# Kernel tuning notes

Hardware: AMD Instinct MI355X
Metric: run time of the kernel (lower is better)

## Reference

```python
import jax, jax.numpy as jnp
import numpy as np

N = 50000          # total particles (nodes)
E = 800000         # num edges
D = 256            # embed_dim
H = 8              # num_heads
ED = 6             # edge_dim
HD = D // H // 2   # head_dim = 16
LAMBDA_INIT = 1.0 - float(np.exp(-1.0))  # lambda_init_fn(depth=1)


def setup_inputs() -> dict:
    key = jax.random.key(0)
    ks = jax.random.split(key, 9)
    sc = lambda k, shape, fan_in: jax.random.normal(k, shape, jnp.float32) * (fan_in ** -0.5)
    x = jax.random.normal(ks[0], (N, D), jnp.float32)
    edge_index = jax.random.randint(ks[1], (2, E), 0, N, dtype=jnp.int64)
    edge_attr = jax.random.normal(ks[2], (E, ED), jnp.float32)
    v_w = sc(ks[3], (D, D), D)
    out_w = sc(ks[4], (D, D), D)
    e_w1 = sc(ks[5], (D, ED), ED)
    e_b1 = jnp.zeros((D,), jnp.float32)
    e_w2 = sc(ks[6], (2 * H, D), D)
    e_b2 = jnp.zeros((2 * H,), jnp.float32)
    lambda_q1 = 0.1 * jax.random.normal(ks[7], (100,), jnp.float32)
    lambda_k1 = 0.1 * jax.random.normal(ks[8], (100,), jnp.float32)
    return {"x": x, "edge_attr": edge_attr, "v_w": v_w, "out_w": out_w,
            "e_w1": e_w1, "e_b1": e_b1, "e_w2": e_w2, "e_b2": e_b2,
            "lambda_q1": lambda_q1, "lambda_k1": lambda_k1,
            "edge_index": edge_index}


def _scatter_softmax(scores, tgt, n):
    # numerically-stable segment softmax over edges grouped by tgt node
    m = jax.ops.segment_max(scores, tgt, num_segments=n)      # [n, H]
    e = jnp.exp(scores - m[tgt])                              # [E, H]
    s = jax.ops.segment_sum(e, tgt, num_segments=n)           # [n, H]
    return e / s[tgt]


def reference(x, edge_attr, v_w, out_w, e_w1, e_b1, e_w2, e_b2,
              lambda_q1, lambda_k1, edge_index):
    src, tgt = edge_index[0], edge_index[1]
    # V projection (no bias), split into heads of size 2*head_dim
    V = (x @ v_w.T).reshape(N, H, 2 * HD)
    # edge encoder MLP: Linear -> GELU(exact) -> Linear
    h = jax.nn.gelu(edge_attr @ e_w1.T + e_b1, approximate=False)
    edge_scores = (h @ e_w2.T + e_b2).reshape(E, H, 2)
    a1 = _scatter_softmax(edge_scores[:, :, 0], tgt, N)
    a2 = _scatter_softmax(edge_scores[:, :, 1], tgt, N)
    lambda_1 = jnp.exp(jnp.sum(lambda_q1 * lambda_k1))
    beta = jax.nn.sigmoid(lambda_1 * LAMBDA_INIT)
    attn_weights = a1 - beta * a2                              # [E, H]
    weighted_V = attn_weights[:, :, None] * V[src]             # [E, H, 2*HD]
    out = jax.ops.segment_sum(weighted_V, tgt, num_segments=N).reshape(N, D)
    out = out @ out_w.T
    return out, attn_weights, beta
```

## Files before the change

### kernel.cpp

```cpp
#include <hip/hip_runtime.h>
#include <hip/hip_bf16.h>
#include <math.h>

#define N_NODES 50000
#define N_EDGES 800000
#define DIM 256
#define HEADS 8
#define LAMBDA_INIT 0.63212055882855767f

using bf16x8 = __attribute__((ext_vector_type(8))) short;
using bf16x4 = __attribute__((ext_vector_type(4))) short;
using f32x4  = __attribute__((ext_vector_type(4))) float;
using f32x2  = __attribute__((ext_vector_type(2))) float;
#define MFMA16(a, b, c) __builtin_amdgcn_mfma_f32_16x16x32_bf16(a, b, c, 0, 0, 0)

__device__ __forceinline__ short f2b(float f) {
    __hip_bfloat16 h = __float2bfloat16(f);
    return *reinterpret_cast<short*>(&h);
}
__device__ __forceinline__ float b2f(short s) {
    unsigned u = ((unsigned)(unsigned short)s) << 16;
    return __uint_as_float(u);
}
__device__ __forceinline__ unsigned cvt_pk_bf16(float a, float b) {
    unsigned r;
    asm("v_cvt_pk_bf16_f32 %0, %1, %2" : "=v"(r) : "v"(a), "v"(b));
    return r;
}

__device__ __forceinline__ float gelu_f(float x) {
    float az = 0.70710678118654752f * fabsf(x);
    float t  = __builtin_amdgcn_rcpf(fmaf(0.47047f, az, 1.f));
    float q  = fmaf(fmaf(0.3739278f, t, -0.0479399f), t, 0.1740121f) * t;
    float E  = __expf(-az * az);
    return fmaf(-q * E, fabsf(x), fmaxf(x, 0.f));
}

__global__ __launch_bounds__(256) void scan1(const int* __restrict__ cnt,
                                             int* __restrict__ offs,
                                             int* __restrict__ partials, int n) {
    __shared__ int sh[256];
    int i = blockIdx.x * 256 + threadIdx.x;
    int v = (i < n) ? cnt[i] : 0;
    sh[threadIdx.x] = v;
    __syncthreads();
    for (int s = 1; s < 256; s <<= 1) {
        int add = (threadIdx.x >= s) ? sh[threadIdx.x - s] : 0;
        __syncthreads();
        sh[threadIdx.x] += add;
        __syncthreads();
    }
    if (i < n) offs[i] = sh[threadIdx.x] - v;
    if (threadIdx.x == 255) partials[blockIdx.x] = sh[255];
}

__global__ __launch_bounds__(256) void scan2(int* __restrict__ partials, int nb,
                                             const float* __restrict__ lq,
                                             const float* __restrict__ lk,
                                             float* __restrict__ beta_ws,
                                             float* __restrict__ beta_out) {
    __shared__ int sh[256];
    __shared__ float redb[128];
    int tid = threadIdx.x;
    int v = (tid < nb) ? partials[tid] : 0;
    sh[tid] = v;
    __syncthreads();
    for (int s = 1; s < 256; s <<= 1) {
        int add = (tid >= s) ? sh[tid - s] : 0;
        __syncthreads();
        sh[tid] += add;
        __syncthreads();
    }
    if (tid < nb) partials[tid] = sh[tid] - v;

    if (tid < 128) {
        float b = 0.f;
        for (int i = tid; i < 100; i += 128) b += lq[i] * lk[i];
        redb[tid] = b;
    }
    __syncthreads();
    for (int s = 64; s > 0; s >>= 1) {
        if (tid < s) redb[tid] += redb[tid + s];
        __syncthreads();
    }
    if (tid == 0) {
        float l1 = expf(redb[0]);
        float b = 1.f / (1.f + expf(-l1 * LAMBDA_INIT));
        *beta_ws = b;
        *beta_out = b;
    }
}

__global__ __launch_bounds__(256) void scan3(int* __restrict__ offs,
                                             const int* __restrict__ partials,
                                             int* __restrict__ cursor, int n) {
    int i = blockIdx.x * 256 + threadIdx.x;
    if (i < n) {
        int o = offs[i] + partials[blockIdx.x];
        offs[i] = o;
        cursor[i] = o;
    }
    if (i == 0) offs[n] = N_EDGES;
}

__global__ __launch_bounds__(256) void scatter_eid(const int* __restrict__ tgt,
                                                   int* __restrict__ cursor,
                                                   int* __restrict__ sorted_eid) {
    int e = blockIdx.x * 256 + threadIdx.x;
    if (e < N_EDGES) {
        int p = atomicAdd(&cursor[tgt[e]], 1);
        sorted_eid[p] = e;
    }
}

template <bool ABF, bool CBF>
__global__ __launch_bounds__(256) void gemm_mfma_t(const void* __restrict__ Av,
                                                   const float* __restrict__ W,
                                                   void* __restrict__ Cv, int M) {
    __shared__ __align__(16) short As[128 * 40];
    __shared__ __align__(16) short Ws[64 * 40];
    int tid = threadIdx.x;
    int lane = tid & 63, wv = tid >> 6;
    int l16 = lane & 15, quad = lane >> 4;
    int bm = blockIdx.x * 128, bn = blockIdx.y * 64;

    f32x4 acc[2][4];
#pragma unroll
    for (int mt = 0; mt < 2; ++mt)
#pragma unroll
        for (int nt = 0; nt < 4; ++nt) acc[mt][nt] = (f32x4){0.f, 0.f, 0.f, 0.f};

    int r = tid >> 1, hf = tid & 1;
    int rw = (tid & 127) >> 1, hw = tid & 1;

    for (int k0 = 0; k0 < 256; k0 += 32) {
        {
            int m = bm + r;
            bf16x8 p0, p1;
            if (ABF) {
                if (m < M) {
                    const bf16x8* ap =
                        (const bf16x8*)&((const short*)Av)[(size_t)m * 256 + k0 + hf * 16];
                    p0 = ap[0]; p1 = ap[1];
                } else {
                    p0 = (bf16x8){0,0,0,0,0,0,0,0}; p1 = p0;
                }
            } else {
                float4 f0, f1, f2, f3;
                if (m < M) {
                    const float4* ap =
                        (const float4*)&((const float*)Av)[(size_t)m * 256 + k0 + hf * 16];
                    f0 = ap[0]; f1 = ap[1]; f2 = ap[2]; f3 = ap[3];
                } else {
                    f0 = f1 = f2 = f3 = make_float4(0.f, 0.f, 0.f, 0.f);
                }
                p0[0]=f2b(f0.x); p0[1]=f2b(f0.y); p0[2]=f2b(f0.z); p0[3]=f2b(f0.w);
                p0[4]=f2b(f1.x); p0[5]=f2b(f1.y); p0[6]=f2b(f1.z); p0[7]=f2b(f1.w);
                p1[0]=f2b(f2.x); p1[1]=f2b(f2.y); p1[2]=f2b(f2.z); p1[3]=f2b(f2.w);
                p1[4]=f2b(f3.x); p1[5]=f2b(f3.y); p1[6]=f2b(f3.z); p1[7]=f2b(f3.w);
            }
            *(bf16x8*)&As[r * 40 + hf * 16]     = p0;
            *(bf16x8*)&As[r * 40 + hf * 16 + 8] = p1;
        }
        if (tid < 128) {
            const float4* wp = (const float4*)&W[(size_t)(bn + rw) * 256 + k0 + hw * 16];
            float4 f0 = wp[0], f1 = wp[1], f2 = wp[2], f3 = wp[3];
            bf16x8 p0, p1;
            p0[0]=f2b(f0.x); p0[1]=f2b(f0.y); p0[2]=f2b(f0.z); p0[3]=f2b(f0.w);
            p0[4]=f2b(f1.x); p0[5]=f2b(f1.y); p0[6]=f2b(f1.z); p0[7]=f2b(f1.w);
            p1[0]=f2b(f2.x); p1[1]=f2b(f2.y); p1[2]=f2b(f2.z); p1[3]=f2b(f2.w);
            p1[4]=f2b(f3.x); p1[5]=f2b(f3.y); p1[6]=f2b(f3.z); p1[7]=f2b(f3.w);
            *(bf16x8*)&Ws[rw * 40 + hw * 16]     = p0;
            *(bf16x8*)&Ws[rw * 40 + hw * 16 + 8] = p1;
        }
        __syncthreads();
#pragma unroll
        for (int mt = 0; mt < 2; ++mt) {
            bf16x8 afr = *(bf16x8*)&As[(wv * 32 + mt * 16 + l16) * 40 + quad * 8];
#pragma unroll
            for (int nt = 0; nt < 4; ++nt) {
                bf16x8 bfr = *(bf16x8*)&Ws[(nt * 16 + l16) * 40 + quad * 8];
                acc[mt][nt] = MFMA16(afr, bfr, acc[mt][nt]);
            }
        }
        __syncthreads();
    }
#pragma unroll
    for (int mt = 0; mt < 2; ++mt) {
#pragma unroll
        for (int rr = 0; rr < 4; ++rr) {
            int m = bm + wv * 32 + mt * 16 + quad * 4 + rr;
            if (m < M) {
#pragma unroll
                for (int nt = 0; nt < 4; ++nt) {
                    if (CBF)
                        ((short*)Cv)[(size_t)m * 256 + bn + nt * 16 + l16] =
                            f2b(acc[mt][nt][rr]);
                    else
                        ((float*)Cv)[(size_t)m * 256 + bn + nt * 16 + l16] =
                            acc[mt][nt][rr];
                }
            }
        }
    }
}

__global__ __launch_bounds__(256) void edge_mlp_mfma(const float* __restrict__ edge_attr,
                                                     const float* __restrict__ e_w1,
                                                     const float* __restrict__ e_b1,
                                                     const float* __restrict__ e_w2,
                                                     const float* __restrict__ e_b2,
                                                     float* __restrict__ scores,
                                                     const int* __restrict__ tgt,
                                                     int* __restrict__ cnt) {
    __shared__ __align__(16) short w1s[256 * 8];
    __shared__ __align__(16) float b1s[256];
    __shared__ __align__(16) float ea_s[256 * 6];

    int tid = threadIdx.x;
    int lane = tid & 63, wv = tid >> 6;
    int l16 = lane & 15, quad = lane >> 4;

    atomicAdd(&cnt[tgt[blockIdx.x * 256 + tid]], 1);

    {
        int n = tid;
#pragma unroll
        for (int k = 0; k < 6; ++k) w1s[n * 8 + k] = f2b(e_w1[n * 6 + k]);
        w1s[n * 8 + 6] = 0; w1s[n * 8 + 7] = 0;
        b1s[n] = e_b1[n];
    }
    {
        size_t base = (size_t)blockIdx.x * (256 * 6);
#pragma unroll
        for (int it = 0; it < 6; ++it) {
            int i = tid + it * 256;
            ea_s[i] = edge_attr[base + i];
        }
    }

    bf16x8 w2f[8];
#pragma unroll
    for (int c = 0; c < 8; ++c) {
#pragma unroll
        for (int j = 0; j < 8; ++j) {
            int col = c * 32 + ((j & 4) ? 16 : 0) + quad * 4 + (j & 3);
            w2f[c][j] = f2b(e_w2[l16 * 256 + col]);
        }
    }
    float b2r = e_b2[l16];
    __syncthreads();

    bf16x8 bfr[4];
#pragma unroll
    for (int g = 0; g < 4; ++g) {
        bfr[g] = (bf16x8){0, 0, 0, 0, 0, 0, 0, 0};
        if (quad == 0) {
            const float* p = &ea_s[(wv * 64 + g * 16 + l16) * 6];
#pragma unroll
            for (int j = 0; j < 6; ++j) bfr[g][j] = f2b(p[j]);
        }
    }

    f32x4 acc[4];
#pragma unroll
    for (int g = 0; g < 4; ++g) acc[g] = (f32x4){0.f, 0.f, 0.f, 0.f};

#pragma unroll
    for (int c2 = 0; c2 < 8; ++c2) {
        bf16x8 af0 = (bf16x8){0, 0, 0, 0, 0, 0, 0, 0};
        bf16x8 af1 = (bf16x8){0, 0, 0, 0, 0, 0, 0, 0};
        if (quad == 0) {
            af0 = *(bf16x8*)&w1s[((2 * c2) * 16 + l16) * 8];
            af1 = *(bf16x8*)&w1s[((2 * c2 + 1) * 16 + l16) * 8];
        }
        f32x4 bb0 = *(const f32x4*)&b1s[(2 * c2) * 16 + quad * 4];
        f32x4 bb1 = *(const f32x4*)&b1s[(2 * c2 + 1) * 16 + quad * 4];
#pragma unroll
        for (int g = 0; g < 4; ++g) {
            f32x4 cc0 = MFMA16(af0, bfr[g], bb0);
            f32x4 cc1 = MFMA16(af1, bfr[g], bb1);
            unsigned pw[4];
            pw[0] = cvt_pk_bf16(gelu_f(cc0[0]), gelu_f(cc0[1]));
            pw[1] = cvt_pk_bf16(gelu_f(cc0[2]), gelu_f(cc0[3]));
            pw[2] = cvt_pk_bf16(gelu_f(cc1[0]), gelu_f(cc1[1]));
            pw[3] = cvt_pk_bf16(gelu_f(cc1[2]), gelu_f(cc1[3]));
            bf16x8 pa = *reinterpret_cast<bf16x8*>(pw);
            acc[g] = MFMA16(pa, w2f[c2], acc[g]);
        }
    }

    long eblk = (long)blockIdx.x * 256 + wv * 64;
#pragma unroll
    for (int g = 0; g < 4; ++g) {
        long e0 = eblk + g * 16;
#pragma unroll
        for (int rr = 0; rr < 4; ++rr)
            scores[(size_t)(e0 + quad * 4 + rr) * 16 + l16] = acc[g][rr] + b2r;
    }
}

__global__ __launch_bounds__(256) void node_agg3(const int* __restrict__ sorted_eid,
                                                 const int* __restrict__ offs,
                                                 const int* __restrict__ srcp,
                                                 const float* __restrict__ scores,
                                                 const short* __restrict__ Vb,
                                                 const float* __restrict__ betap,
                                                 short* __restrict__ accumb,
                                                 float* __restrict__ attn_out) {
    __shared__ __align__(16) float scr_all[4][16 * 65];
    __shared__ __align__(16) float ms_all[4][32];
    __shared__ int src_all[4][64];

    int tid = threadIdx.x;
    int wv = tid >> 6, lane = tid & 63;
    int n = blockIdx.x * 4 + wv;
    float* scr = scr_all[wv];
    float* ms  = ms_all[wv];
    int* srcs  = src_all[wv];

    int beg = offs[n];
    int deg = offs[n + 1] - beg;
    int c16 = lane & 15, q4 = lane >> 4;
    int d0 = lane * 4, hh = lane >> 3;

    if (deg == 0) {
        bf16x4 z = (bf16x4){0, 0, 0, 0};
        *(bf16x4*)&accumb[(size_t)n * 256 + d0] = z;
        return;
    }
    float beta = *betap;

    if (deg <= 64) {
        int k = lane;
        int eid = 0, src = 0;
        float sc[16];
        if (k < deg) {
            eid = sorted_eid[beg + k];
            src = srcp[eid];
            const f32x4* sp = (const f32x4*)&scores[(size_t)eid * 16];
            f32x4 s0 = sp[0], s1 = sp[1], s2 = sp[2], s3 = sp[3];
            sc[0]=s0[0]; sc[1]=s0[1]; sc[2]=s0[2]; sc[3]=s0[3];
            sc[4]=s1[0]; sc[5]=s1[1]; sc[6]=s1[2]; sc[7]=s1[3];
            sc[8]=s2[0]; sc[9]=s2[1]; sc[10]=s2[2]; sc[11]=s2[3];
            sc[12]=s3[0]; sc[13]=s3[1]; sc[14]=s3[2]; sc[15]=s3[3];
        } else {
#pragma unroll
            for (int c = 0; c < 16; ++c) sc[c] = -INFINITY;
        }
        srcs[k] = src;
#pragma unroll
        for (int c = 0; c < 16; ++c) scr[c * 65 + k] = sc[c];

        float mloc = -INFINITY;
        for (int j = 0; 4 * j < deg; ++j)
            mloc = fmaxf(mloc, scr[c16 * 65 + 4 * j + q4]);
        mloc = fmaxf(mloc, __shfl_xor(mloc, 16));
        mloc = fmaxf(mloc, __shfl_xor(mloc, 32));
        float sloc = 0.f;
        for (int j = 0; 4 * j < deg; ++j)
            sloc += __expf(scr[c16 * 65 + 4 * j + q4] - mloc);
        sloc += __shfl_xor(sloc, 16);
        sloc += __shfl_xor(sloc, 32);
        if (lane < 16) {
            ms[c16] = mloc;
            ms[16 + c16] = __builtin_amdgcn_rcpf(sloc);
        }

        if (k < deg) {
            float w[8];
#pragma unroll
            for (int h = 0; h < 8; ++h) {
                f32x2 mp = *(const f32x2*)&ms[2 * h];
                f32x2 rp = *(const f32x2*)&ms[16 + 2 * h];
                w[h] = __expf(sc[2 * h] - mp[0]) * rp[0]
                     - beta * __expf(sc[2 * h + 1] - mp[1]) * rp[1];
            }
            f32x4 w0 = (f32x4){w[0], w[1], w[2], w[3]};
            f32x4 w1 = (f32x4){w[4], w[5], w[6], w[7]};
            *(f32x4*)&attn_out[(size_t)eid * 8]     = w0;
            *(f32x4*)&attn_out[(size_t)eid * 8 + 4] = w1;
            *(f32x4*)&scr[k * 8]     = w0;
            *(f32x4*)&scr[k * 8 + 4] = w1;
        }

        float a0 = 0.f, a1 = 0.f, a2 = 0.f, a3 = 0.f;
        for (int kk = 0; kk < deg; ++kk) {
            float wk = scr[kk * 8 + hh];
            int sk = srcs[kk];
            bf16x4 v = *(const bf16x4*)&Vb[(size_t)sk * 256 + d0];
            a0 += wk * b2f(v[0]);
            a1 += wk * b2f(v[1]);
            a2 += wk * b2f(v[2]);
            a3 += wk * b2f(v[3]);
        }
        bf16x4 r;
        r[0] = f2b(a0); r[1] = f2b(a1); r[2] = f2b(a2); r[3] = f2b(a3);
        *(bf16x4*)&accumb[(size_t)n * 256 + d0] = r;
        return;
    }

    float m_run = -INFINITY, s_run = 0.f;
    for (int base = 0; base < deg; base += 64) {
        int k = base + lane;
        float sc[16];
        if (k < deg) {
            int eid = sorted_eid[beg + k];
            const f32x4* sp = (const f32x4*)&scores[(size_t)eid * 16];
            f32x4 s0 = sp[0], s1 = sp[1], s2 = sp[2], s3 = sp[3];
            sc[0]=s0[0]; sc[1]=s0[1]; sc[2]=s0[2]; sc[3]=s0[3];
            sc[4]=s1[0]; sc[5]=s1[1]; sc[6]=s1[2]; sc[7]=s1[3];
            sc[8]=s2[0]; sc[9]=s2[1]; sc[10]=s2[2]; sc[11]=s2[3];
            sc[12]=s3[0]; sc[13]=s3[1]; sc[14]=s3[2]; sc[15]=s3[3];
        } else {
#pragma unroll
            for (int c = 0; c < 16; ++c) sc[c] = -INFINITY;
        }
#pragma unroll
        for (int c = 0; c < 16; ++c) scr[c * 65 + lane] = sc[c];
        float mc = -INFINITY;
#pragma unroll
        for (int j = 0; j < 16; ++j)
            mc = fmaxf(mc, scr[c16 * 65 + 4 * j + q4]);
        mc = fmaxf(mc, __shfl_xor(mc, 16));
        mc = fmaxf(mc, __shfl_xor(mc, 32));
        float m_new = fmaxf(m_run, mc);
        float ssum = 0.f;
#pragma unroll
        for (int j = 0; j < 16; ++j)
            ssum += __expf(scr[c16 * 65 + 4 * j + q4] - m_new);
        ssum += __shfl_xor(ssum, 16);
        ssum += __shfl_xor(ssum, 32);
        s_run = s_run * __expf(m_run - m_new) + ssum;
        m_run = m_new;
    }
    if (lane < 16) {
        ms[c16] = m_run;
        ms[16 + c16] = __builtin_amdgcn_rcpf(s_run);
    }

    float a0 = 0.f, a1 = 0.f, a2 = 0.f, a3 = 0.f;
    for (int base = 0; base < deg; base += 64) {
        int k = base + lane;
        int cn = min(64, deg - base);
        int src = 0;
        if (lane < cn) {
            int eid = sorted_eid[beg + k];
            src = srcp[eid];
            const f32x4* sp = (const f32x4*)&scores[(size_t)eid * 16];
            f32x4 s0 = sp[0], s1 = sp[1], s2 = sp[2], s3 = sp[3];
            float sc[16];
            sc[0]=s0[0]; sc[1]=s0[1]; sc[2]=s0[2]; sc[3]=s0[3];
            sc[4]=s1[0]; sc[5]=s1[1]; sc[6]=s1[2]; sc[7]=s1[3];
            sc[8]=s2[0]; sc[9]=s2[1]; sc[10]=s2[2]; sc[11]=s2[3];
            sc[12]=s3[0]; sc[13]=s3[1]; sc[14]=s3[2]; sc[15]=s3[3];
            float w[8];
#pragma unroll
            for (int h = 0; h < 8; ++h) {
                f32x2 mp = *(const f32x2*)&ms[2 * h];
                f32x2 rp = *(const f32x2*)&ms[16 + 2 * h];
                w[h] = __expf(sc[2 * h] - mp[0]) * rp[0]
                     - beta * __expf(sc[2 * h + 1] - mp[1]) * rp[1];
            }
            f32x4 w0 = (f32x4){w[0], w[1], w[2], w[3]};
            f32x4 w1 = (f32x4){w[4], w[5], w[6], w[7]};
            *(f32x4*)&attn_out[(size_t)eid * 8]     = w0;
            *(f32x4*)&attn_out[(size_t)eid * 8 + 4] = w1;
            *(f32x4*)&scr[lane * 8]     = w0;
            *(f32x4*)&scr[lane * 8 + 4] = w1;
        }
        srcs[lane] = src;
        for (int kk = 0; kk < cn; ++kk) {
            float wk = scr[kk * 8 + hh];
            int sk = srcs[kk];
            bf16x4 v = *(const bf16x4*)&Vb[(size_t)sk * 256 + d0];
            a0 += wk * b2f(v[0]);
            a1 += wk * b2f(v[1]);
            a2 += wk * b2f(v[2]);
            a3 += wk * b2f(v[3]);
        }
    }
    bf16x4 r;
    r[0] = f2b(a0); r[1] = f2b(a1); r[2] = f2b(a2); r[3] = f2b(a3);
    *(bf16x4*)&accumb[(size_t)n * 256 + d0] = r;
}

extern "C" void kernel_launch(void* const* d_in, const int* in_sizes, int n_in,
                              void* d_out, int out_size, void* d_ws, size_t ws_size,
                              hipStream_t stream) {
    const float* x         = (const float*)d_in[0];
    const float* edge_attr = (const float*)d_in[1];
    const float* v_w       = (const float*)d_in[2];
    const float* out_w     = (const float*)d_in[3];
    const float* e_w1      = (const float*)d_in[4];
    const float* e_b1      = (const float*)d_in[5];
    const float* e_w2      = (const float*)d_in[6];
    const float* e_b2      = (const float*)d_in[7];
    const float* lq        = (const float*)d_in[8];
    const float* lk        = (const float*)d_in[9];
    const int*   ei        = (const int*)d_in[10];
    const int* srcp = ei;
    const int* tgtp = ei + N_EDGES;

    float* out = (float*)d_out;
    float* attn_out = out + (size_t)N_NODES * 256;
    float* beta_out = attn_out + (size_t)N_EDGES * 8;

    short* Vb     = (short*)d_ws;
    float* scores = (float*)(Vb + (size_t)N_NODES * 256);
    short* accumb = (short*)(scores + (size_t)N_EDGES * 16);
    int*   cnt    = (int*)(accumb + (size_t)N_NODES * 256);
    int*   offs   = cnt + N_NODES;
    int*   cursor = offs + N_NODES + 1;
    int*   partials = cursor + N_NODES;
    int*   sorted_eid = partials + 256;
    float* betap  = (float*)(sorted_eid + N_EDGES);

    const int NB = (N_NODES + 255) / 256;

    hipMemsetAsync(cnt, 0, N_NODES * sizeof(int), stream);

    edge_mlp_mfma<<<N_EDGES / 256, 256, 0, stream>>>(edge_attr, e_w1, e_b1, e_w2, e_b2,
                                                     scores, tgtp, cnt);

    scan1<<<NB, 256, 0, stream>>>(cnt, offs, partials, N_NODES);
    scan2<<<1, 256, 0, stream>>>(partials, NB, lq, lk, betap, beta_out);
    scan3<<<NB, 256, 0, stream>>>(offs, partials, cursor, N_NODES);
    scatter_eid<<<(N_EDGES + 255) / 256, 256, 0, stream>>>(tgtp, cursor, sorted_eid);

    gemm_mfma_t<false, true><<<dim3((N_NODES + 127) / 128, 4), 256, 0, stream>>>(
        x, v_w, Vb, N_NODES);

    node_agg3<<<N_NODES / 4, 256, 0, stream>>>(sorted_eid, offs, srcp, scores, Vb, betap,
                                               accumb, attn_out);

    gemm_mfma_t<true, false><<<dim3((N_NODES + 127) / 128, 4), 256, 0, stream>>>(
        accumb, out_w, out, N_NODES);
}
```

Baseline: 459.5 us.

## Fuse edge counting into V GEMM and scatter scores directly into sorted slots

The target-degree histogram moves into the V projection GEMM. The edge MLP now runs after the prefix scan, claims each edge's sorted slot with an atomic cursor, and writes its scores, edge id and source index straight into slot order. This removes the separate scatter_eid kernel and lets the aggregation kernel read scores and sources contiguously instead of through an eid indirection. The cost is scattered 64-byte score writes from the MLP kernel and an extra slot_src array.

```diff
diff --git a/kernel.cpp b/kernel.cpp
--- a/kernel.cpp
+++ b/kernel.cpp
@@ -103,26 +103,25 @@
     if (i == 0) offs[n] = N_EDGES;
 }
 
-__global__ __launch_bounds__(256) void scatter_eid(const int* __restrict__ tgt,
-                                                   int* __restrict__ cursor,
-                                                   int* __restrict__ sorted_eid) {
-    int e = blockIdx.x * 256 + threadIdx.x;
-    if (e < N_EDGES) {
-        int p = atomicAdd(&cursor[tgt[e]], 1);
-        sorted_eid[p] = e;
-    }
-}
-
 template <bool ABF, bool CBF>
 __global__ __launch_bounds__(256) void gemm_mfma_t(const void* __restrict__ Av,
                                                    const float* __restrict__ W,
-                                                   void* __restrict__ Cv, int M) {
+                                                   void* __restrict__ Cv, int M,
+                                                   const int* __restrict__ hist_tgt,
+                                                   int* __restrict__ hist_cnt) {
     __shared__ __align__(16) short As[128 * 40];
     __shared__ __align__(16) short Ws[64 * 40];
     int tid = threadIdx.x;
     int lane = tid & 63, wv = tid >> 6;
     int l16 = lane & 15, quad = lane >> 4;
     int bm = blockIdx.x * 128, bn = blockIdx.y * 64;
+
+    if (hist_tgt) {
+        int gtid = (blockIdx.x * 4 + blockIdx.y) * 256 + tid;
+        int e0 = gtid * 2;
+        if (e0 < N_EDGES)     atomicAdd(&hist_cnt[hist_tgt[e0]], 1);
+        if (e0 + 1 < N_EDGES) atomicAdd(&hist_cnt[hist_tgt[e0 + 1]], 1);
+    }
 
     f32x4 acc[2][4];
 #pragma unroll
@@ -210,18 +209,29 @@
                                                      const float* __restrict__ e_b1,
                                                      const float* __restrict__ e_w2,
                                                      const float* __restrict__ e_b2,
-                                                     float* __restrict__ scores,
                                                      const int* __restrict__ tgt,
-                                                     int* __restrict__ cnt) {
+                                                     const int* __restrict__ srcp,
+                                                     int* __restrict__ cursor,
+                                                     float* __restrict__ sorted_sc,
+                                                     int* __restrict__ slot_eid,
+                                                     int* __restrict__ slot_src) {
     __shared__ __align__(16) short w1s[256 * 8];
     __shared__ __align__(16) float b1s[256];
     __shared__ __align__(16) float ea_s[256 * 6];
+    __shared__ int slot_lds[4][64];
 
     int tid = threadIdx.x;
     int lane = tid & 63, wv = tid >> 6;
     int l16 = lane & 15, quad = lane >> 4;
-
-    atomicAdd(&cnt[tgt[blockIdx.x * 256 + tid]], 1);
+    long eblk = (long)blockIdx.x * 256 + wv * 64;
+
+    {
+        int e = (int)(eblk + lane);
+        int p = atomicAdd(&cursor[tgt[e]], 1);
+        slot_lds[wv][lane] = p;
+        slot_eid[p] = e;
+        slot_src[p] = srcp[e];
+    }
 
     {
         int n = tid;
@@ -290,20 +300,20 @@
         }
     }
 
-    long eblk = (long)blockIdx.x * 256 + wv * 64;
 #pragma unroll
     for (int g = 0; g < 4; ++g) {
-        long e0 = eblk + g * 16;
-#pragma unroll
-        for (int rr = 0; rr < 4; ++rr)
-            scores[(size_t)(e0 + quad * 4 + rr) * 16 + l16] = acc[g][rr] + b2r;
-    }
-}
-
-__global__ __launch_bounds__(256) void node_agg3(const int* __restrict__ sorted_eid,
+#pragma unroll
+        for (int rr = 0; rr < 4; ++rr) {
+            int p = slot_lds[wv][g * 16 + quad * 4 + rr];
+            sorted_sc[(size_t)p * 16 + l16] = acc[g][rr] + b2r;
+        }
+    }
+}
+
+__global__ __launch_bounds__(256) void node_agg4(const int* __restrict__ slot_eid,
                                                  const int* __restrict__ offs,
-                                                 const int* __restrict__ srcp,
-                                                 const float* __restrict__ scores,
+                                                 const int* __restrict__ slot_src,
+                                                 const float* __restrict__ sorted_sc,
                                                  const short* __restrict__ Vb,
                                                  const float* __restrict__ betap,
                                                  short* __restrict__ accumb,
@@ -336,9 +346,10 @@
         int eid = 0, src = 0;
         float sc[16];
         if (k < deg) {
-            eid = sorted_eid[beg + k];
-            src = srcp[eid];
-            const f32x4* sp = (const f32x4*)&scores[(size_t)eid * 16];
+            int slot = beg + k;
+            eid = slot_eid[slot];
+            src = slot_src[slot];
+            const f32x4* sp = (const f32x4*)&sorted_sc[(size_t)slot * 16];
             f32x4 s0 = sp[0], s1 = sp[1], s2 = sp[2], s3 = sp[3];
             sc[0]=s0[0]; sc[1]=s0[1]; sc[2]=s0[2]; sc[3]=s0[3];
             sc[4]=s1[0]; sc[5]=s1[1]; sc[6]=s1[2]; sc[7]=s1[3];
@@ -405,8 +416,7 @@
         int k = base + lane;
         float sc[16];
         if (k < deg) {
-            int eid = sorted_eid[beg + k];
-            const f32x4* sp = (const f32x4*)&scores[(size_t)eid * 16];
+            const f32x4* sp = (const f32x4*)&sorted_sc[(size_t)(beg + k) * 16];
             f32x4 s0 = sp[0], s1 = sp[1], s2 = sp[2], s3 = sp[3];
             sc[0]=s0[0]; sc[1]=s0[1]; sc[2]=s0[2]; sc[3]=s0[3];
             sc[4]=s1[0]; sc[5]=s1[1]; sc[6]=s1[2]; sc[7]=s1[3];
@@ -445,9 +455,10 @@
         int cn = min(64, deg - base);
         int src = 0;
         if (lane < cn) {
-            int eid = sorted_eid[beg + k];
-            src = srcp[eid];
-            const f32x4* sp = (const f32x4*)&scores[(size_t)eid * 16];
+            int slot = beg + k;
+            int eid = slot_eid[slot];
+            src = slot_src[slot];
+            const f32x4* sp = (const f32x4*)&sorted_sc[(size_t)slot * 16];
             f32x4 s0 = sp[0], s1 = sp[1], s2 = sp[2], s3 = sp[3];
             float sc[16];
             sc[0]=s0[0]; sc[1]=s0[1]; sc[2]=s0[2]; sc[3]=s0[3];
@@ -506,34 +517,35 @@
     float* attn_out = out + (size_t)N_NODES * 256;
     float* beta_out = attn_out + (size_t)N_EDGES * 8;
 
-    short* Vb     = (short*)d_ws;
-    float* scores = (float*)(Vb + (size_t)N_NODES * 256);
-    short* accumb = (short*)(scores + (size_t)N_EDGES * 16);
-    int*   cnt    = (int*)(accumb + (size_t)N_NODES * 256);
-    int*   offs   = cnt + N_NODES;
-    int*   cursor = offs + N_NODES + 1;
+    short* Vb       = (short*)d_ws;
+    float* sorted_sc= (float*)(Vb + (size_t)N_NODES * 256);
+    short* accumb   = (short*)(sorted_sc + (size_t)N_EDGES * 16);
+    int*   cnt      = (int*)(accumb + (size_t)N_NODES * 256);
+    int*   offs     = cnt + N_NODES;
+    int*   cursor   = offs + N_NODES + 1;
     int*   partials = cursor + N_NODES;
-    int*   sorted_eid = partials + 256;
-    float* betap  = (float*)(sorted_eid + N_EDGES);
+    int*   slot_eid = partials + 256;
+    int*   slot_src = slot_eid + N_EDGES;
+    float* betap    = (float*)(slot_src + N_EDGES);
 
     const int NB = (N_NODES + 255) / 256;
 
     hipMemsetAsync(cnt, 0, N_NODES * sizeof(int), stream);
 
-    edge_mlp_mfma<<<N_EDGES / 256, 256, 0, stream>>>(edge_attr, e_w1, e_b1, e_w2, e_b2,
-                                                     scores, tgtp, cnt);
+    gemm_mfma_t<false, true><<<dim3((N_NODES + 127) / 128, 4), 256, 0, stream>>>(
+        x, v_w, Vb, N_NODES, tgtp, cnt);
 
     scan1<<<NB, 256, 0, stream>>>(cnt, offs, partials, N_NODES);
     scan2<<<1, 256, 0, stream>>>(partials, NB, lq, lk, betap, beta_out);
     scan3<<<NB, 256, 0, stream>>>(offs, partials, cursor, N_NODES);
-    scatter_eid<<<(N_EDGES + 255) / 256, 256, 0, stream>>>(tgtp, cursor, sorted_eid);
-
-    gemm_mfma_t<false, true><<<dim3((N_NODES + 127) / 128, 4), 256, 0, stream>>>(
-        x, v_w, Vb, N_NODES);
-
-    node_agg3<<<N_NODES / 4, 256, 0, stream>>>(sorted_eid, offs, srcp, scores, Vb, betap,
-                                               accumb, attn_out);
+
+    edge_mlp_mfma<<<N_EDGES / 256, 256, 0, stream>>>(edge_attr, e_w1, e_b1, e_w2, e_b2,
+                                                     tgtp, srcp, cursor,
+                                                     sorted_sc, slot_eid, slot_src);
+
+    node_agg4<<<N_NODES / 4, 256, 0, stream>>>(slot_eid, offs, slot_src, sorted_sc,
+                                               Vb, betap, accumb, attn_out);
 
     gemm_mfma_t<true, false><<<dim3((N_NODES + 127) / 128, 4), 256, 0, stream>>>(
-        accumb, out_w, out, N_NODES);
-}
+        accumb, out_w, out, N_NODES, nullptr, nullptr);
+}
```

New measurement: 421.0 us. 1.09x faster.
